# Performance work log

Measured on AMD Instinct MI355X. Metric: run time of the kernel, lower is better.

## Reference

```python
import jax, jax.numpy as jnp
import numpy as np

K = 3
STRIDE = 1
PAD = 1


def _conv(x, w, b):
    y = jax.lax.conv_general_dilated(
        x, w, window_strides=(STRIDE, STRIDE),
        padding=[(PAD, PAD), (PAD, PAD)],
        dimension_numbers=('NCHW', 'OIHW', 'NCHW'))
    return y + b[None, :, None, None]


def setup_inputs() -> dict:
    key = jax.random.key(0)
    ks = jax.random.split(key, 6)
    B, Cin, H, W = 4, 64, 128, 128
    Cout = 128
    x = jax.random.normal(ks[0], (B, Cin, H, W), dtype=jnp.float32)
    # small random offset/mask conv params (original inits to 0, which would be degenerate)
    w_off = jax.random.normal(ks[1], (2 * K * K, Cin, K, K), dtype=jnp.float32) * 0.01
    b_off = jax.random.normal(ks[2], (2 * K * K,), dtype=jnp.float32) * 0.1
    w_mask = jax.random.normal(ks[3], (K * K, Cin, K, K), dtype=jnp.float32) * 0.01
    b_mask = jnp.zeros((K * K,), dtype=jnp.float32)
    # kaiming_uniform(a=sqrt(5)) -> bound = 1/sqrt(fan_in)
    fan_in = Cin * K * K
    bound = 1.0 / np.sqrt(fan_in)
    weight = jax.random.uniform(ks[4], (Cout, Cin, K, K), dtype=jnp.float32,
                                minval=-bound, maxval=bound)
    return {"x": x, "w_off": w_off, "b_off": b_off,
            "w_mask": w_mask, "b_mask": b_mask, "weight": weight}


def _deform_conv(x, offset, mask, weight):
    B, C, H, W = x.shape
    O = weight.shape[0]
    KK = K * K
    Ho, Wo = offset.shape[2], offset.shape[3]
    # torchvision layout: offset[:, 2k] = dy_k, offset[:, 2k+1] = dx_k
    off = offset.reshape(B, KK, 2, Ho, Wo)
    dy, dx = off[:, :, 0], off[:, :, 1]  # [B,KK,Ho,Wo]

    ky, kx = jnp.meshgrid(jnp.arange(K), jnp.arange(K), indexing='ij')
    ky = ky.reshape(KK).astype(jnp.float32)
    kx = kx.reshape(KK).astype(jnp.float32)
    oy = jnp.arange(Ho, dtype=jnp.float32) * STRIDE - PAD
    ox = jnp.arange(Wo, dtype=jnp.float32) * STRIDE - PAD
    # sampling positions [B,KK,Ho,Wo]
    py = oy[None, None, :, None] + ky[None, :, None, None] + dy
    px = ox[None, None, None, :] + kx[None, :, None, None] + dx

    y0 = jnp.floor(py)
    x0 = jnp.floor(px)
    ly = py - y0
    lx = px - x0
    y0i = y0.astype(jnp.int32)
    x0i = x0.astype(jnp.int32)

    x_flat = x.reshape(B, C, H * W)
    gather = jax.vmap(lambda xf, idx: xf[:, idx])  # ([C,HW],[KK,Ho,Wo])->[C,KK,Ho,Wo]

    def corner(yi, xi, wgt):
        valid = ((yi >= 0) & (yi < H) & (xi >= 0) & (xi < W)).astype(x.dtype)
        yc = jnp.clip(yi, 0, H - 1)
        xc = jnp.clip(xi, 0, W - 1)
        g = gather(x_flat, yc * W + xc)  # [B,C,KK,Ho,Wo]
        return g * (wgt * valid)[:, None]

    sampled = (corner(y0i, x0i, (1 - ly) * (1 - lx))
               + corner(y0i, x0i + 1, (1 - ly) * lx)
               + corner(y0i + 1, x0i, ly * (1 - lx))
               + corner(y0i + 1, x0i + 1, ly * lx))  # [B,C,KK,Ho,Wo]

    sampled = sampled * mask[:, None]  # modulation, mask [B,KK,Ho,Wo]
    w = weight.reshape(O, C, KK)
    return jnp.einsum('bckhw,ock->bohw', sampled, w)


def reference(x, w_off, b_off, w_mask, b_mask, weight):
    offset = _conv(x, w_off, b_off)
    mask = jax.nn.sigmoid(_conv(x, w_mask, b_mask))
    return _deform_conv(x, offset, mask, weight)
```

## Files before the change

### kernel.cpp

```cpp
#include <hip/hip_runtime.h>
#include <math.h>

#define B 4
#define CIN 64
#define H 128
#define W 128
#define COUT 128
#define KK 9
#define HW (H*W)

#define OFFS_SZ (B*18*HW)
#define MASK_SZ (B*9*HW)
#define WBF_COLS 640
#define WBF_SHORTS (COUT*WBF_COLS)
#define WCV_SHORTS (32*640)
#define LDK 168

typedef __attribute__((ext_vector_type(8))) short short8;
typedef __attribute__((ext_vector_type(4))) float f32x4;
typedef __attribute__((ext_vector_type(2))) float f32x2;
typedef f32x2 __attribute__((aligned(4))) f32x2a;

#define GLDS16(g, l) __builtin_amdgcn_global_load_lds(                        \
    (__attribute__((address_space(1))) void*)(g),                             \
    (__attribute__((address_space(3))) void*)(l), 16, 0, 0)

__device__ __forceinline__ unsigned short f2bf(float f) {
    unsigned int u = __float_as_uint(f);
    u += 0x7fffu + ((u >> 16) & 1u);
    return (unsigned short)(u >> 16);
}

__global__ void prep_wcv(const float* __restrict__ w_off, const float* __restrict__ b_off,
                         const float* __restrict__ w_mask, const float* __restrict__ b_mask,
                         short* __restrict__ wcv, float* __restrict__ bcat)
{
    int idx = blockIdx.x * 256 + threadIdx.x;
    if (idx < WCV_SHORTS) {
        int f  = idx / 640;
        int kp = idx % 640;
        int cb = kp / 160, r = kp % 160;
        float v = 0.f;
        if (r < 144) {
            int tap = r >> 4;
            int c   = cb * 16 + (r & 15);
            if (f < 18)      v = w_off[(f * CIN + c) * 9 + tap];
            else if (f < 27) v = w_mask[((f - 18) * CIN + c) * 9 + tap];
        }
        wcv[idx] = (short)f2bf(v);
    }
    if (blockIdx.x == 0 && threadIdx.x < 32) {
        int f = threadIdx.x;
        float bv = 0.f;
        if (f < 18) bv = b_off[f];
        else if (f < 27) bv = b_mask[f - 18];
        bcat[f] = bv;
    }
}

__global__ void prep_wbf(const float* __restrict__ wgt, short* __restrict__ wbf)
{
    int idx = blockIdx.x * 256 + threadIdx.x;
    if (idx >= WBF_SHORTS) return;
    int o  = idx / WBF_COLS;
    int kp = idx % WBF_COLS;
    int cb = kp / 160, r = kp % 160;
    float v = 0.f;
    if (r < 144) {
        int tap = r >> 4;
        int c   = cb * 16 + (r & 15);
        v = wgt[(o * CIN + c) * KK + tap];
    }
    wbf[idx] = (short)f2bf(v);
}


__global__ __launch_bounds__(256, 2) void offmask6_kernel(
    const float* __restrict__ x, const short* __restrict__ wcv,
    const float* __restrict__ bcat, float* __restrict__ offs,
    float* __restrict__ mask)
{
    const int bid = blockIdx.x;
    const int T = (bid & 7) * 128 + (bid >> 3);
    const int wo0 = (T & 1) * 64;
    const int ho  = (T >> 1) & 127;
    const int b   = T >> 8;
    const int tid  = threadIdx.x;
    const int lane = tid & 63;
    const int wv   = tid >> 6;
    const int row16 = lane & 15, kq = lane >> 4;

    __shared__ __align__(16) float XW3[8 * 3 * 72];
    __shared__ __align__(16) short S2[64 * LDK];

    if (tid < 128) {
        short8 z = {0,0,0,0,0,0,0,0};
        *(short8*)&S2[(tid >> 1) * LDK + 144 + (tid & 1) * 8] = z;
    }

    const float* xb = x + (size_t)b * CIN * HW;

    int st_goff[2];
    #pragma unroll
    for (int t = 0; t < 2; ++t) {
        int idx = tid + t * 256;
        int ci = idx / 54, rem = idx % 54, row = rem / 18, q = rem % 18;
        int ys = min(max(ho - 1 + row, 0), H - 1);
        int g0 = wo0 - 4 + q * 4;
        int g0c = min(max(g0, 0), W - 4);
        st_goff[t] = ci * HW + ys * W + g0c;
    }
    auto stage = [&](int h) {
        const float* base = xb + (size_t)h * 8 * HW;
        #pragma unroll
        for (int t = 0; t < 2; ++t) {
            if (tid + t * 256 < 432) {
                GLDS16(base + st_goff[t], &XW3[(tid + t * 256) * 4]);
            }
        }
    };

    int bidx[3];
    #pragma unroll
    for (int j = 0; j < 3; ++j) {
        bidx[j] = -1;
        int s = tid + j * 256;
        if (s < 576) {
            int k = s >> 6, p = s & 63;
            int ky = k / 3, kx = k % 3;
            bool ok = ((unsigned)(ho - 1 + ky) < (unsigned)H)
                   && ((unsigned)(wo0 + p - 1 + kx) < (unsigned)W);
            if (ok) bidx[j] = ky * 72 + (p + 3 + kx);
        }
    }

    f32x4 acc2[2];
    acc2[0] = (f32x4){0.f, 0.f, 0.f, 0.f};
    acc2[1] = (f32x4){0.f, 0.f, 0.f, 0.f};

    auto build = [&](int h) {
        #pragma unroll
        for (int j = 0; j < 3; ++j) {
            int s = tid + j * 256;
            if (s < 576) {
                int k = s >> 6, p = s & 63;
                short8 sv = {0,0,0,0,0,0,0,0};
                if (bidx[j] >= 0) {
                    #pragma unroll
                    for (int ci = 0; ci < 8; ++ci)
                        sv[ci] = (short)f2bf(XW3[ci * 216 + bidx[j]]);
                }
                *(short8*)&S2[p * LDK + k * 16 + (h & 1) * 8] = sv;
            }
        }
    };

    auto mfma_off = [&](int c) {
        #pragma unroll
        for (int ks = 0; ks < 5; ++ks) {
            short8 a0 = *(const short8*)(wcv + (row16)      * 640 + c * 160 + ks * 32 + kq * 8);
            short8 a1 = *(const short8*)(wcv + (16 + row16) * 640 + c * 160 + ks * 32 + kq * 8);
            short8 bfr = *(const short8*)&S2[(wv * 16 + row16) * LDK + ks * 32 + kq * 8];
            acc2[0] = __builtin_amdgcn_mfma_f32_16x16x32_bf16(a0, bfr, acc2[0], 0, 0, 0);
            acc2[1] = __builtin_amdgcn_mfma_f32_16x16x32_bf16(a1, bfr, acc2[1], 0, 0, 0);
        }
    };

    stage(0); __syncthreads(); build(0); __syncthreads();
    stage(1); __syncthreads(); build(1); __syncthreads();
    #pragma unroll 1
    for (int c = 0; c < 3; ++c) {
        stage(2 * c + 2);
        mfma_off(c);
        __syncthreads();
        build(2 * c + 2);
        __syncthreads();
        stage(2 * c + 3);
        __syncthreads();
        build(2 * c + 3);
        __syncthreads();
    }
    mfma_off(3);

    const int px = wo0 + wv * 16 + row16;
    #pragma unroll
    for (int of = 0; of < 2; ++of) {
        #pragma unroll
        for (int r = 0; r < 4; ++r) {
            int f = of * 16 + kq * 4 + r;
            if (f < 27) {
                float v = acc2[of][r] + bcat[f];
                if (f < 18) {
                    offs[((b * 18 + f) * H + ho) * W + px] = v;
                } else {
                    mask[((b * 9 + (f - 18)) * H + ho) * W + px] =
                        1.f / (1.f + expf(-v));
                }
            }
        }
    }
}

__global__ __launch_bounds__(256, 2) void deform8_kernel(
    const float* __restrict__ x, const float* __restrict__ offs,
    const float* __restrict__ maskp, const short* __restrict__ wbf,
    float* __restrict__ out)
{
    const int bid = blockIdx.x;
    const int T = (bid & 7) * 128 + (bid >> 3);
    const int wo0 = (T & 1) * 64;
    const int ho  = (T >> 1) & 127;
    const int b   = T >> 8;
    const int tid  = threadIdx.x;
    const int lane = tid & 63;
    const int wv   = tid >> 6;
    const int oh   = (wv & 1) * 64;
    const int ph   = (wv >> 1) * 32;
    const int row16 = lane & 15, kq = lane >> 4;

    __shared__ __align__(16) float XW[8 * 6 * 72];
    __shared__ __align__(16) short S[64 * LDK];

    if (tid < 128) {
        short8 z = {0,0,0,0,0,0,0,0};
        *(short8*)&S[(tid >> 1) * LDK + 144 + (tid & 1) * 8] = z;
    }

    const float* xb = x + (size_t)b * CIN * HW;

    int st_goff[4];
    #pragma unroll
    for (int t = 0; t < 4; ++t) {
        int idx = tid + t * 256;
        int ci = idx / 108, rem = idx % 108, row = rem / 18, q = rem % 18;
        int ys = min(max(ho - 2 + row, 0), H - 1);
        int g0 = wo0 - 4 + q * 4;
        int g0c = min(max(g0, 0), W - 4);
        st_goff[t] = ci * HW + ys * W + g0c;
    }
    auto stage = [&](int h) {
        const float* base = xb + (size_t)h * 8 * HW;
        #pragma unroll
        for (int t = 0; t < 4; ++t) {
            if (tid + t * 256 < 864) {
                GLDS16(base + st_goff[t], &XW[(tid + t * 256) * 4]);
            }
        }
    };

    int   moff[3][2];
    int   lidx0[3], lidx1[3];
    float wA0[3], wB0[3], wA1[3], wB1[3];
    #pragma unroll
    for (int j = 0; j < 3; ++j) {
        moff[j][0] = 0; moff[j][1] = 0;
        lidx0[j] = -1; lidx1[j] = 0;
        wA0[j] = 0.f; wB0[j] = 0.f; wA1[j] = 0.f; wB1[j] = 0.f;
        int s = tid + j * 256;
        if (s < 576) {
            int k = s >> 6, p = s & 63;
            int wo = wo0 + p;
            int ky = k / 3, kx = k % 3;
            int obase = ((b * 18 + 2 * k) * H + ho) * W + wo;
            float dy = offs[obase];
            float dx = offs[obase + HW];
            float mk = maskp[((b * 9 + k) * H + ho) * W + wo];
            float py  = (float)(ho - 1 + ky) + dy;
            float pxf = (float)(wo - 1 + kx) + dx;
            float fy = floorf(py), fx = floorf(pxf);
            float ly = py - fy, lx = pxf - fx;
            int y0 = (int)fy, x0 = (int)fx;
            int y1 = y0 + 1,  x1 = x0 + 1;
            bool vy0 = (y0 >= 0) && (y0 < H);
            bool vy1 = (y1 >= 0) && (y1 < H);
            bool vx0 = (x0 >= 0) && (x0 < W);
            bool vx1 = (x1 >= 0) && (x1 < W);
            float w0 = (vy0 && vx0) ? (1.f - ly) * (1.f - lx) * mk : 0.f;
            float w1 = (vy0 && vx1) ? (1.f - ly) * lx * mk : 0.f;
            float w2 = (vy1 && vx0) ? ly * (1.f - lx) * mk : 0.f;
            float w3 = (vy1 && vx1) ? ly * lx * mk : 0.f;
            int lc = min(max(x0, 0), W - 2);
            bool sel = (x0 == lc);
            int r0 = min(max(y0, 0), H - 1);
            int r1 = min(max(y1, 0), H - 1);
            moff[j][0] = (r0 * W + lc) * 4;
            moff[j][1] = (r1 * W + lc) * 4;
            wA0[j] = sel ? w0 : w1;  wB0[j] = sel ? w1 : w0;
            wA1[j] = sel ? w2 : w3;  wB1[j] = sel ? w3 : w2;
            int u0 = r0 - (ho - 2);
            int u1 = r1 - (ho - 2);
            int vvv = lc - (wo0 - 4);
            bool fastp = ((unsigned)u0 < 6u) && ((unsigned)u1 < 6u)
                       && ((unsigned)vvv < 71u);
            lidx1[j] = u1 * 72 + vvv;
            lidx0[j] = fastp ? (u0 * 72 + vvv) : -1;
        }
    }

    f32x4 acc[4][2];
    #pragma unroll
    for (int i = 0; i < 4; ++i)
        #pragma unroll
        for (int j = 0; j < 2; ++j)
            acc[i][j] = (f32x4){0.f, 0.f, 0.f, 0.f};

    auto sample = [&](int h) {
        #pragma unroll
        for (int j = 0; j < 3; ++j) {
            int s = tid + j * 256;
            if (s < 576) {
                int k = s >> 6, p = s & 63;
                float va[8];
                float wa0 = wA0[j], wb0 = wB0[j], wa1 = wA1[j], wb1 = wB1[j];
                if (lidx0[j] >= 0) {
                    int l0 = lidx0[j], l1 = lidx1[j];
                    #pragma unroll
                    for (int ci = 0; ci < 8; ++ci) {
                        const float* bp = &XW[ci * 432];
                        f32x2 A  = *(const f32x2a*)(bp + l0);
                        f32x2 Bv = *(const f32x2a*)(bp + l1);
                        va[ci] = wa0 * A.x + wb0 * A.y + wa1 * Bv.x + wb1 * Bv.y;
                    }
                } else {
                    #pragma unroll
                    for (int ci = 0; ci < 8; ++ci) {
                        const char* pc = (const char*)(xb + (size_t)(h * 8 + ci) * HW);
                        f32x2 A  = *(const f32x2a*)(pc + moff[j][0]);
                        f32x2 Bv = *(const f32x2a*)(pc + moff[j][1]);
                        va[ci] = wa0 * A.x + wb0 * A.y + wa1 * Bv.x + wb1 * Bv.y;
                    }
                }
                short8 sv;
                #pragma unroll
                for (int ci = 0; ci < 8; ++ci) sv[ci] = (short)f2bf(va[ci]);
                *(short8*)&S[p * LDK + k * 16 + (h & 1) * 8] = sv;
            }
        }
    };

    auto mfma_step = [&](int c) {
        #pragma unroll
        for (int ks = 0; ks < 5; ++ks) {
            short8 a[4];
            #pragma unroll
            for (int of = 0; of < 4; ++of) {
                int o = oh + of * 16 + row16;
                a[of] = *(const short8*)(wbf + o * WBF_COLS + c * 160 + ks * 32 + kq * 8);
            }
            #pragma unroll
            for (int pf = 0; pf < 2; ++pf) {
                int p = ph + pf * 16 + row16;
                short8 bfr = *(const short8*)&S[p * LDK + ks * 32 + kq * 8];
                #pragma unroll
                for (int of = 0; of < 4; ++of)
                    acc[of][pf] = __builtin_amdgcn_mfma_f32_16x16x32_bf16(
                        a[of], bfr, acc[of][pf], 0, 0, 0);
            }
        }
    };

    stage(0); __syncthreads(); sample(0); __syncthreads();
    stage(1); __syncthreads(); sample(1); __syncthreads();
    #pragma unroll 1
    for (int c = 0; c < 3; ++c) {
        stage(2 * c + 2);
        mfma_step(c);
        __syncthreads();
        sample(2 * c + 2);
        __syncthreads();
        stage(2 * c + 3);
        __syncthreads();
        sample(2 * c + 3);
        __syncthreads();
    }
    mfma_step(3);

    #pragma unroll
    for (int of = 0; of < 4; ++of) {
        #pragma unroll
        for (int r = 0; r < 4; ++r) {
            int o = oh + of * 16 + kq * 4 + r;
            float* orow = out + ((b * COUT + o) * H + ho) * W;
            #pragma unroll
            for (int pf = 0; pf < 2; ++pf) {
                int wo = wo0 + ph + pf * 16 + row16;
                orow[wo] = acc[of][pf][r];
            }
        }
    }
}

extern "C" void kernel_launch(void* const* d_in, const int* in_sizes, int n_in,
                              void* d_out, int out_size, void* d_ws, size_t ws_size,
                              hipStream_t stream)
{
    const float* x      = (const float*)d_in[0];
    const float* w_off  = (const float*)d_in[1];
    const float* b_off  = (const float*)d_in[2];
    const float* w_mask = (const float*)d_in[3];
    const float* b_mask = (const float*)d_in[4];
    const float* weight = (const float*)d_in[5];
    float* out   = (float*)d_out;

    float* offs  = (float*)d_ws;
    float* maskb = offs + OFFS_SZ;
    float* bcat  = maskb + MASK_SZ;
    short* wbf   = (short*)(bcat + 32);
    short* wcv   = wbf + WBF_SHORTS;

    prep_wcv<<<dim3((WCV_SHORTS + 255) / 256), 256, 0, stream>>>(
        w_off, b_off, w_mask, b_mask, wcv, bcat);
    prep_wbf<<<dim3((WBF_SHORTS + 255) / 256), 256, 0, stream>>>(weight, wbf);
    offmask6_kernel<<<dim3(1024), 256, 0, stream>>>(x, wcv, bcat, offs, maskb);
    deform8_kernel<<<dim3(1024), 256, 0, stream>>>(x, offs, maskb, wbf, out);
}
```

Before: 90.95 us.

## Fuse offset/mask conv into deformable conv kernel, keeping offsets in LDS

Merges the offset/mask convolution kernel into the deformable sampling kernel. Each block now computes its row tile's offsets and sigmoid mask into shared memory (aliased on the S buffer), then reuses that shared memory for the deformable GEMM. This drops one kernel launch and the global round trip for the offset and mask tensors. In exchange each block runs both phases in sequence with extra barriers, so there is less cross-block overlap. The bilinear weights are also packed into float2 vectors so the interpolation can use paired multiplies.

```diff
diff --git a/kernel.cpp b/kernel.cpp
--- a/kernel.cpp
+++ b/kernel.cpp
@@ -9,8 +9,6 @@
 #define KK 9
 #define HW (H*W)
 
-#define OFFS_SZ (B*18*HW)
-#define MASK_SZ (B*9*HW)
 #define WBF_COLS 640
 #define WBF_SHORTS (COUT*WBF_COLS)
 #define WCV_SHORTS (32*640)
@@ -74,136 +72,9 @@
     wbf[idx] = (short)f2bf(v);
 }
 
-
-__global__ __launch_bounds__(256, 2) void offmask6_kernel(
+__global__ __launch_bounds__(256, 2) void fused2_kernel(
     const float* __restrict__ x, const short* __restrict__ wcv,
-    const float* __restrict__ bcat, float* __restrict__ offs,
-    float* __restrict__ mask)
-{
-    const int bid = blockIdx.x;
-    const int T = (bid & 7) * 128 + (bid >> 3);
-    const int wo0 = (T & 1) * 64;
-    const int ho  = (T >> 1) & 127;
-    const int b   = T >> 8;
-    const int tid  = threadIdx.x;
-    const int lane = tid & 63;
-    const int wv   = tid >> 6;
-    const int row16 = lane & 15, kq = lane >> 4;
-
-    __shared__ __align__(16) float XW3[8 * 3 * 72];
-    __shared__ __align__(16) short S2[64 * LDK];
-
-    if (tid < 128) {
-        short8 z = {0,0,0,0,0,0,0,0};
-        *(short8*)&S2[(tid >> 1) * LDK + 144 + (tid & 1) * 8] = z;
-    }
-
-    const float* xb = x + (size_t)b * CIN * HW;
-
-    int st_goff[2];
-    #pragma unroll
-    for (int t = 0; t < 2; ++t) {
-        int idx = tid + t * 256;
-        int ci = idx / 54, rem = idx % 54, row = rem / 18, q = rem % 18;
-        int ys = min(max(ho - 1 + row, 0), H - 1);
-        int g0 = wo0 - 4 + q * 4;
-        int g0c = min(max(g0, 0), W - 4);
-        st_goff[t] = ci * HW + ys * W + g0c;
-    }
-    auto stage = [&](int h) {
-        const float* base = xb + (size_t)h * 8 * HW;
-        #pragma unroll
-        for (int t = 0; t < 2; ++t) {
-            if (tid + t * 256 < 432) {
-                GLDS16(base + st_goff[t], &XW3[(tid + t * 256) * 4]);
-            }
-        }
-    };
-
-    int bidx[3];
-    #pragma unroll
-    for (int j = 0; j < 3; ++j) {
-        bidx[j] = -1;
-        int s = tid + j * 256;
-        if (s < 576) {
-            int k = s >> 6, p = s & 63;
-            int ky = k / 3, kx = k % 3;
-            bool ok = ((unsigned)(ho - 1 + ky) < (unsigned)H)
-                   && ((unsigned)(wo0 + p - 1 + kx) < (unsigned)W);
-            if (ok) bidx[j] = ky * 72 + (p + 3 + kx);
-        }
-    }
-
-    f32x4 acc2[2];
-    acc2[0] = (f32x4){0.f, 0.f, 0.f, 0.f};
-    acc2[1] = (f32x4){0.f, 0.f, 0.f, 0.f};
-
-    auto build = [&](int h) {
-        #pragma unroll
-        for (int j = 0; j < 3; ++j) {
-            int s = tid + j * 256;
-            if (s < 576) {
-                int k = s >> 6, p = s & 63;
-                short8 sv = {0,0,0,0,0,0,0,0};
-                if (bidx[j] >= 0) {
-                    #pragma unroll
-                    for (int ci = 0; ci < 8; ++ci)
-                        sv[ci] = (short)f2bf(XW3[ci * 216 + bidx[j]]);
-                }
-                *(short8*)&S2[p * LDK + k * 16 + (h & 1) * 8] = sv;
-            }
-        }
-    };
-
-    auto mfma_off = [&](int c) {
-        #pragma unroll
-        for (int ks = 0; ks < 5; ++ks) {
-            short8 a0 = *(const short8*)(wcv + (row16)      * 640 + c * 160 + ks * 32 + kq * 8);
-            short8 a1 = *(const short8*)(wcv + (16 + row16) * 640 + c * 160 + ks * 32 + kq * 8);
-            short8 bfr = *(const short8*)&S2[(wv * 16 + row16) * LDK + ks * 32 + kq * 8];
-            acc2[0] = __builtin_amdgcn_mfma_f32_16x16x32_bf16(a0, bfr, acc2[0], 0, 0, 0);
-            acc2[1] = __builtin_amdgcn_mfma_f32_16x16x32_bf16(a1, bfr, acc2[1], 0, 0, 0);
-        }
-    };
-
-    stage(0); __syncthreads(); build(0); __syncthreads();
-    stage(1); __syncthreads(); build(1); __syncthreads();
-    #pragma unroll 1
-    for (int c = 0; c < 3; ++c) {
-        stage(2 * c + 2);
-        mfma_off(c);
-        __syncthreads();
-        build(2 * c + 2);
-        __syncthreads();
-        stage(2 * c + 3);
-        __syncthreads();
-        build(2 * c + 3);
-        __syncthreads();
-    }
-    mfma_off(3);
-
-    const int px = wo0 + wv * 16 + row16;
-    #pragma unroll
-    for (int of = 0; of < 2; ++of) {
-        #pragma unroll
-        for (int r = 0; r < 4; ++r) {
-            int f = of * 16 + kq * 4 + r;
-            if (f < 27) {
-                float v = acc2[of][r] + bcat[f];
-                if (f < 18) {
-                    offs[((b * 18 + f) * H + ho) * W + px] = v;
-                } else {
-                    mask[((b * 9 + (f - 18)) * H + ho) * W + px] =
-                        1.f / (1.f + expf(-v));
-                }
-            }
-        }
-    }
-}
-
-__global__ __launch_bounds__(256, 2) void deform8_kernel(
-    const float* __restrict__ x, const float* __restrict__ offs,
-    const float* __restrict__ maskp, const short* __restrict__ wbf,
+    const short* __restrict__ wbf, const float* __restrict__ bcat,
     float* __restrict__ out)
 {
     const int bid = blockIdx.x;
@@ -220,15 +91,50 @@
 
     __shared__ __align__(16) float XW[8 * 6 * 72];
     __shared__ __align__(16) short S[64 * LDK];
+    float* offs_l = (float*)S;
+
+    const float* xb = x + (size_t)b * CIN * HW;
+
+    int stA_goff[2];
+    #pragma unroll
+    for (int t = 0; t < 2; ++t) {
+        int idx = tid + t * 256;
+        int ci = idx / 54, rem = idx % 54, row = rem / 18, q = rem % 18;
+        int ys = min(max(ho - 1 + row, 0), H - 1);
+        int g0 = wo0 - 4 + q * 4;
+        int g0c = min(max(g0, 0), W - 4);
+        stA_goff[t] = ci * HW + ys * W + g0c;
+    }
+    auto stageA = [&](int h) {
+        const float* base = xb + (size_t)h * 8 * HW;
+        #pragma unroll
+        for (int t = 0; t < 2; ++t) {
+            if (tid + t * 256 < 432) {
+                GLDS16(base + stA_goff[t], &XW[(tid + t * 256) * 4]);
+            }
+        }
+    };
 
     if (tid < 128) {
         short8 z = {0,0,0,0,0,0,0,0};
         *(short8*)&S[(tid >> 1) * LDK + 144 + (tid & 1) * 8] = z;
     }
-
-    const float* xb = x + (size_t)b * CIN * HW;
-
-    int st_goff[4];
+    stageA(0);
+
+    int bidx[3];
+    #pragma unroll
+    for (int j = 0; j < 3; ++j) {
+        bidx[j] = -1;
+        int s = tid + j * 256;
+        if (s < 576) {
+            int k = s >> 6, p = s & 63;
+            int ky = k / 3, kx = k % 3;
+            bool ok = ((unsigned)(ho - 1 + ky) < (unsigned)H)
+                   && ((unsigned)(wo0 + p - 1 + kx) < (unsigned)W);
+            if (ok) bidx[j] = ky * 72 + (p + 3 + kx);
+        }
+    }
+    int stB_goff[4];
     #pragma unroll
     for (int t = 0; t < 4; ++t) {
         int idx = tid + t * 256;
@@ -236,35 +142,103 @@
         int ys = min(max(ho - 2 + row, 0), H - 1);
         int g0 = wo0 - 4 + q * 4;
         int g0c = min(max(g0, 0), W - 4);
-        st_goff[t] = ci * HW + ys * W + g0c;
-    }
-    auto stage = [&](int h) {
+        stB_goff[t] = ci * HW + ys * W + g0c;
+    }
+    __syncthreads();
+
+    f32x4 acc2[2];
+    acc2[0] = (f32x4){0.f, 0.f, 0.f, 0.f};
+    acc2[1] = (f32x4){0.f, 0.f, 0.f, 0.f};
+
+    auto buildA = [&](int h) {
+        #pragma unroll
+        for (int j = 0; j < 3; ++j) {
+            int s = tid + j * 256;
+            if (s < 576) {
+                int k = s >> 6, p = s & 63;
+                short8 sv = {0,0,0,0,0,0,0,0};
+                if (bidx[j] >= 0) {
+                    #pragma unroll
+                    for (int ci = 0; ci < 8; ++ci)
+                        sv[ci] = (short)f2bf(XW[ci * 216 + bidx[j]]);
+                }
+                *(short8*)&S[p * LDK + k * 16 + (h & 1) * 8] = sv;
+            }
+        }
+    };
+    auto mfmaA = [&](int c) {
+        #pragma unroll
+        for (int ks = 0; ks < 5; ++ks) {
+            short8 a0 = *(const short8*)(wcv + (row16)      * 640 + c * 160 + ks * 32 + kq * 8);
+            short8 a1 = *(const short8*)(wcv + (16 + row16) * 640 + c * 160 + ks * 32 + kq * 8);
+            short8 bfr = *(const short8*)&S[(wv * 16 + row16) * LDK + ks * 32 + kq * 8];
+            acc2[0] = __builtin_amdgcn_mfma_f32_16x16x32_bf16(a0, bfr, acc2[0], 0, 0, 0);
+            acc2[1] = __builtin_amdgcn_mfma_f32_16x16x32_bf16(a1, bfr, acc2[1], 0, 0, 0);
+        }
+    };
+
+    buildA(0); __syncthreads();
+    stageA(1); __syncthreads(); buildA(1); __syncthreads();
+    #pragma unroll 1
+    for (int c = 0; c < 3; ++c) {
+        stageA(2 * c + 2);
+        mfmaA(c);
+        __syncthreads();
+        buildA(2 * c + 2);
+        __syncthreads();
+        stageA(2 * c + 3);
+        __syncthreads();
+        buildA(2 * c + 3);
+        __syncthreads();
+    }
+    mfmaA(3);
+    __syncthreads();
+
+    {
+        const int pxl = wv * 16 + row16;
+        #pragma unroll
+        for (int of = 0; of < 2; ++of) {
+            #pragma unroll
+            for (int r = 0; r < 4; ++r) {
+                int f = of * 16 + kq * 4 + r;
+                if (f < 27) {
+                    float v = acc2[of][r] + bcat[f];
+                    if (f >= 18) v = 1.f / (1.f + expf(-v));
+                    offs_l[f * 64 + pxl] = v;
+                }
+            }
+        }
+    }
+    __syncthreads();
+
+    auto stageB = [&](int h) {
         const float* base = xb + (size_t)h * 8 * HW;
         #pragma unroll
         for (int t = 0; t < 4; ++t) {
             if (tid + t * 256 < 864) {
-                GLDS16(base + st_goff[t], &XW[(tid + t * 256) * 4]);
-            }
-        }
-    };
+                GLDS16(base + stB_goff[t], &XW[(tid + t * 256) * 4]);
+            }
+        }
+    };
+
+    stageB(0);
 
     int   moff[3][2];
     int   lidx0[3], lidx1[3];
-    float wA0[3], wB0[3], wA1[3], wB1[3];
+    f32x2 wAB[3], wCD[3];
     #pragma unroll
     for (int j = 0; j < 3; ++j) {
         moff[j][0] = 0; moff[j][1] = 0;
         lidx0[j] = -1; lidx1[j] = 0;
-        wA0[j] = 0.f; wB0[j] = 0.f; wA1[j] = 0.f; wB1[j] = 0.f;
+        wAB[j] = (f32x2){0.f, 0.f}; wCD[j] = (f32x2){0.f, 0.f};
         int s = tid + j * 256;
         if (s < 576) {
             int k = s >> 6, p = s & 63;
             int wo = wo0 + p;
             int ky = k / 3, kx = k % 3;
-            int obase = ((b * 18 + 2 * k) * H + ho) * W + wo;
-            float dy = offs[obase];
-            float dx = offs[obase + HW];
-            float mk = maskp[((b * 9 + k) * H + ho) * W + wo];
+            float dy = offs_l[(2 * k) * 64 + p];
+            float dx = offs_l[(2 * k + 1) * 64 + p];
+            float mk = offs_l[(18 + k) * 64 + p];
             float py  = (float)(ho - 1 + ky) + dy;
             float pxf = (float)(wo - 1 + kx) + dx;
             float fy = floorf(py), fx = floorf(pxf);
@@ -285,8 +259,8 @@
             int r1 = min(max(y1, 0), H - 1);
             moff[j][0] = (r0 * W + lc) * 4;
             moff[j][1] = (r1 * W + lc) * 4;
-            wA0[j] = sel ? w0 : w1;  wB0[j] = sel ? w1 : w0;
-            wA1[j] = sel ? w2 : w3;  wB1[j] = sel ? w3 : w2;
+            wAB[j].x = sel ? w0 : w1;  wAB[j].y = sel ? w1 : w0;
+            wCD[j].x = sel ? w2 : w3;  wCD[j].y = sel ? w3 : w2;
             int u0 = r0 - (ho - 2);
             int u1 = r1 - (ho - 2);
             int vvv = lc - (wo0 - 4);
@@ -296,6 +270,12 @@
             lidx0[j] = fastp ? (u0 * 72 + vvv) : -1;
         }
     }
+    __syncthreads();
+
+    if (tid < 128) {
+        short8 z = {0,0,0,0,0,0,0,0};
+        *(short8*)&S[(tid >> 1) * LDK + 144 + (tid & 1) * 8] = z;
+    }
 
     f32x4 acc[4][2];
     #pragma unroll
@@ -304,14 +284,14 @@
         for (int j = 0; j < 2; ++j)
             acc[i][j] = (f32x4){0.f, 0.f, 0.f, 0.f};
 
-    auto sample = [&](int h) {
+    auto sampleB = [&](int h) {
         #pragma unroll
         for (int j = 0; j < 3; ++j) {
             int s = tid + j * 256;
             if (s < 576) {
                 int k = s >> 6, p = s & 63;
                 float va[8];
-                float wa0 = wA0[j], wb0 = wB0[j], wa1 = wA1[j], wb1 = wB1[j];
+                f32x2 wab = wAB[j], wcd = wCD[j];
                 if (lidx0[j] >= 0) {
                     int l0 = lidx0[j], l1 = lidx1[j];
                     #pragma unroll
@@ -319,7 +299,8 @@
                         const float* bp = &XW[ci * 432];
                         f32x2 A  = *(const f32x2a*)(bp + l0);
                         f32x2 Bv = *(const f32x2a*)(bp + l1);
-                        va[ci] = wa0 * A.x + wb0 * A.y + wa1 * Bv.x + wb1 * Bv.y;
+                        f32x2 t = A * wab + Bv * wcd;
+                        va[ci] = t.x + t.y;
                     }
                 } else {
                     #pragma unroll
@@ -327,7 +308,8 @@
                         const char* pc = (const char*)(xb + (size_t)(h * 8 + ci) * HW);
                         f32x2 A  = *(const f32x2a*)(pc + moff[j][0]);
                         f32x2 Bv = *(const f32x2a*)(pc + moff[j][1]);
-                        va[ci] = wa0 * A.x + wb0 * A.y + wa1 * Bv.x + wb1 * Bv.y;
+                        f32x2 t = A * wab + Bv * wcd;
+                        va[ci] = t.x + t.y;
                     }
                 }
                 short8 sv;
@@ -338,7 +320,7 @@
         }
     };
 
-    auto mfma_step = [&](int c) {
+    auto mfmaB = [&](int c) {
         #pragma unroll
         for (int ks = 0; ks < 5; ++ks) {
             short8 a[4];
@@ -359,21 +341,21 @@
         }
     };
 
-    stage(0); __syncthreads(); sample(0); __syncthreads();
-    stage(1); __syncthreads(); sample(1); __syncthreads();
+    sampleB(0); __syncthreads();
+    stageB(1); __syncthreads(); sampleB(1); __syncthreads();
     #pragma unroll 1
     for (int c = 0; c < 3; ++c) {
-        stage(2 * c + 2);
-        mfma_step(c);
-        __syncthreads();
-        sample(2 * c + 2);
-        __syncthreads();
-        stage(2 * c + 3);
-        __syncthreads();
-        sample(2 * c + 3);
-        __syncthreads();
-    }
-    mfma_step(3);
+        stageB(2 * c + 2);
+        mfmaB(c);
+        __syncthreads();
+        sampleB(2 * c + 2);
+        __syncthreads();
+        stageB(2 * c + 3);
+        __syncthreads();
+        sampleB(2 * c + 3);
+        __syncthreads();
+    }
+    mfmaB(3);
 
     #pragma unroll
     for (int of = 0; of < 4; ++of) {
@@ -402,15 +384,12 @@
     const float* weight = (const float*)d_in[5];
     float* out   = (float*)d_out;
 
-    float* offs  = (float*)d_ws;
-    float* maskb = offs + OFFS_SZ;
-    float* bcat  = maskb + MASK_SZ;
+    float* bcat  = (float*)d_ws;
     short* wbf   = (short*)(bcat + 32);
     short* wcv   = wbf + WBF_SHORTS;
 
     prep_wcv<<<dim3((WCV_SHORTS + 255) / 256), 256, 0, stream>>>(
         w_off, b_off, w_mask, b_mask, wcv, bcat);
     prep_wbf<<<dim3((WBF_SHORTS + 255) / 256), 256, 0, stream>>>(weight, wbf);
-    offmask6_kernel<<<dim3(1024), 256, 0, stream>>>(x, wcv, bcat, offs, maskb);
-    deform8_kernel<<<dim3(1024), 256, 0, stream>>>(x, offs, maskb, wbf, out);
-}
+    fused2_kernel<<<dim3(1024), 256, 0, stream>>>(x, wcv, wbf, bcat, out);
+}
```

After: 84.71 us. -6.9%, faster.
